# Kernel optimization log

Measured on AMD Instinct MI355X. Metric: run time of the kernel, lower is better.

The kernel has to match this reference:

```python
import jax, jax.numpy as jnp
import numpy as np

N_HEAD, D_HEAD = 10, 38
D_MODEL, D_INNER = 380, 900
QLEN, BSZ = 1024, 4
MIN_LEN, MAX_LEN = -1024, 1024
EPS = 1e-5
SCALE = 1.0 / D_HEAD ** 0.5


def _ln(x, g, b):
    m = x.mean(-1, keepdims=True)
    v = ((x - m) ** 2).mean(-1, keepdims=True)
    return (x - m) / jnp.sqrt(v + EPS) * g + b


def setup_inputs() -> dict:
    key = jax.random.key(0)
    ks = jax.random.split(key, 10)
    s = 0.02
    w = jax.random.normal(ks[0], (QLEN, BSZ, D_MODEL), jnp.float32)
    # sinusoidal relative position embeddings over positions max_len .. min_len
    pos = jnp.arange(MAX_LEN, MIN_LEN - 1, -1, dtype=jnp.float32)  # [rlen]
    inv_freq = 1.0 / (10000.0 ** (jnp.arange(0, D_MODEL, 2, dtype=jnp.float32) / D_MODEL))
    sin_inp = pos[:, None] * inv_freq[None, :]
    r = jnp.concatenate([jnp.sin(sin_inp), jnp.cos(sin_inp)], axis=-1)  # [rlen, d_model]
    # causal mask, True = attend; layout [qlen, klen, bsz]
    attn_mask = jnp.broadcast_to(jnp.tril(jnp.ones((QLEN, QLEN), bool))[:, :, None], (QLEN, QLEN, BSZ))
    attn_relpos = jax.random.randint(ks[1], (BSZ, QLEN, QLEN), MIN_LEN, MAX_LEN + 1).astype(jnp.int32)
    return {
        'w': w,
        'r': r,
        'r_w_bias': s * jax.random.normal(ks[2], (N_HEAD, D_HEAD), jnp.float32),
        'r_r_bias': s * jax.random.normal(ks[3], (N_HEAD, D_HEAD), jnp.float32),
        'qkv_w': s * jax.random.normal(ks[4], (3 * N_HEAD * D_HEAD, D_MODEL), jnp.float32),
        'r_w': s * jax.random.normal(ks[5], (N_HEAD * D_HEAD, D_MODEL), jnp.float32),
        'o_w': s * jax.random.normal(ks[6], (D_MODEL, N_HEAD * D_HEAD), jnp.float32),
        'ln1_g': jnp.ones(D_MODEL, jnp.float32), 'ln1_b': jnp.zeros(D_MODEL, jnp.float32),
        'ff_w1': s * jax.random.normal(ks[7], (D_INNER, D_MODEL), jnp.float32),
        'ff_b1': jnp.zeros(D_INNER, jnp.float32),
        'ff_w2': s * jax.random.normal(ks[8], (D_MODEL, D_INNER), jnp.float32),
        'ff_b2': jnp.zeros(D_MODEL, jnp.float32),
        'ln2_g': jnp.ones(D_MODEL, jnp.float32), 'ln2_b': jnp.zeros(D_MODEL, jnp.float32),
        'attn_mask': attn_mask,
        'attn_relpos': attn_relpos,
        'min_len': MIN_LEN,
        'max_len': MAX_LEN,
    }


def reference(w, r, r_w_bias, r_r_bias, qkv_w, r_w, o_w, ln1_g, ln1_b,
              ff_w1, ff_b1, ff_w2, ff_b2, ln2_g, ln2_b,
              attn_mask, attn_relpos, min_len, max_len):
    qlen, bsz, _ = w.shape
    # qkv projection (no mems, post-lnorm)
    heads = jnp.einsum('ibm,hm->ibh', w, qkv_w)  # [q, b, 3*nh*dh]
    q, k, v = jnp.split(heads, 3, axis=-1)
    q = q.reshape(qlen, bsz, N_HEAD, D_HEAD)
    k = k.reshape(qlen, bsz, N_HEAD, D_HEAD)
    v = v.reshape(qlen, bsz, N_HEAD, D_HEAD)
    rk = (r @ r_w.T).reshape(-1, N_HEAD, D_HEAD)  # [rlen, nh, dh]
    # content score AC and position score BD (Transformer-XL)
    AC = jnp.einsum('ibnd,jbnd->ijbn', q + r_w_bias, k)   # [q, k, b, n]
    BD = jnp.einsum('ibnd,jnd->ijbn', q + r_r_bias, rk)   # [q, rlen, b, n]
    # gather-based relative position indexing (attn_relpos path)
    idx = (max_len - jnp.clip(attn_relpos, min_len, max_len)).transpose(1, 2, 0)  # [q, k, b]
    idx4 = jnp.broadcast_to(idx[..., None], idx.shape + (N_HEAD,))
    BD = jnp.take_along_axis(BD, idx4, axis=1)            # [q, k, b, n]
    score = (AC + BD) * SCALE
    score = jnp.where(attn_mask[:, :, :, None], score, -jnp.inf)
    prob = jax.nn.softmax(score, axis=1)
    vec = jnp.einsum('ijbn,jbnd->ibnd', prob, v).reshape(qlen, bsz, N_HEAD * D_HEAD)
    attn_out = vec @ o_w.T
    out = _ln(w + attn_out, ln1_g, ln1_b)
    # position-wise FF, post-lnorm
    core = jax.nn.relu(out @ ff_w1.T + ff_b1) @ ff_w2.T + ff_b2
    return _ln(out + core, ln2_g, ln2_b)
```

## Files before the change

kernel.cpp:

```cpp
#include <hip/hip_runtime.h>
#include <math.h>

#define QLEN 1024
#define BSZ 4
#define NH 10
#define DH 38
#define DM 380
#define DI 900
#define H3 1140
#define RLEN 2049
#define RLP 2112
#define SCALE 0.16222142113076254f

typedef unsigned short ushortt;
typedef __attribute__((ext_vector_type(8))) short short8;
typedef __attribute__((ext_vector_type(4))) float float4v;

__device__ __forceinline__ float bf2f(ushortt u) {
    return __uint_as_float(((unsigned int)u) << 16);
}
__device__ __forceinline__ ushortt f2bf(float f) {
    unsigned int u = __float_as_uint(f);
    u += 0x7fffu + ((u >> 16) & 1u);
    return (ushortt)(u >> 16);
}

__device__ __forceinline__ void convseg(const float* src, ushortt* dst,
                                        int R, int C, int Rp, int Cp,
                                        int tid0, int stride) {
    const int total = Rp * Cp;
    for (int i = tid0; i < total; i += stride) {
        int r = i / Cp, c = i - r * Cp;
        float v = (r < R && c < C) ? src[(size_t)r * C + c] : 0.f;
        dst[i] = f2bf(v);
    }
}

__global__ __launch_bounds__(256)
void prep_all(const float* __restrict__ w,    ushortt* __restrict__ w_bf,
              const float* __restrict__ qkv,  ushortt* __restrict__ qkv_bf,
              const float* __restrict__ r,    ushortt* __restrict__ r_bf,
              const float* __restrict__ rw,   ushortt* __restrict__ rw_bf,
              const float* __restrict__ ow,   ushortt* __restrict__ ow_bf,
              const float* __restrict__ f1,   ushortt* __restrict__ f1_bf,
              const float* __restrict__ f2,   ushortt* __restrict__ f2_bf,
              ushortt* __restrict__ qw_bf, ushortt* __restrict__ Kb, ushortt* __restrict__ Vb,
              ushortt* __restrict__ qr_bf, ushortt* __restrict__ rk_bf,
              ushortt* __restrict__ vec) {
    const int stride = gridDim.x * 256;
    const int tid0 = blockIdx.x * 256 + threadIdx.x;
    convseg(w,   w_bf,   4096, DM, 4096, 384, tid0, stride);
    convseg(qkv, qkv_bf, H3,   DM, 1152, 384, tid0, stride);
    convseg(r,   r_bf,   RLEN, DM, 2176, 384, tid0, stride);
    convseg(rw,  rw_bf,  DM,   DM, 384,  384, tid0, stride);
    convseg(ow,  ow_bf,  DM,   DM, 384,  384, tid0, stride);
    convseg(f1,  f1_bf,  DI,   DM, 960,  384, tid0, stride);
    convseg(f2,  f2_bf,  DM,   DI, 384,  928, tid0, stride);
    for (int i = tid0; i < BSZ * NH * 1024 * 2; i += stride) {
        size_t idx = (size_t)(i >> 1) * 40 + 38 + (i & 1);
        Kb[idx] = 0; Vb[idx] = 0;
    }
    for (int i = tid0; i < 4096 * 4; i += stride)
        vec[(size_t)(i >> 2) * 384 + 380 + (i & 3)] = 0;
    for (int i = tid0; i < BSZ * NH * 1024 * 26; i += stride) {
        int row = i / 26, c = 38 + i % 26;
        qr_bf[(size_t)row * 64 + c] = 0;
        qw_bf[(size_t)row * 64 + c] = 0;
    }
    for (int i = tid0; i < NH * RLP * 26; i += stride) {
        int row = i / 26, c = 38 + i % 26;
        rk_bf[(size_t)row * 64 + c] = 0;
    }
    for (int i = tid0; i < NH * 63 * 64; i += stride) {
        int n = i / (63 * 64), rem = i % (63 * 64);
        rk_bf[((size_t)n * RLP + RLEN + rem / 64) * 64 + rem % 64] = 0;
    }
}

template<int EPI>
__global__ __launch_bounds__(256)
void gemm_mfma(const ushortt* __restrict__ A, const ushortt* __restrict__ B,
               const float* __restrict__ bias, void* __restrict__ Cout,
               int M, int N, int Kpp, int ldc,
               const float* __restrict__ bias2, float* __restrict__ out2,
               float* __restrict__ out3, float* __restrict__ out4) {
    __shared__ __align__(16) ushortt As[128 * 32];
    __shared__ __align__(16) ushortt Bs[64 * 32];
    const int tid = threadIdx.x;
    const int wid = tid >> 6, lane = tid & 63;
    const int bRow = blockIdx.y * 128, bCol = blockIdx.x * 64;

    float4v acc[2][4];
    const float4v zz = {0.f, 0.f, 0.f, 0.f};
    #pragma unroll
    for (int m = 0; m < 2; ++m)
        #pragma unroll
        for (int n = 0; n < 4; ++n) acc[m][n] = zz;

    const int arow = tid >> 1, acol = (tid & 1) * 16;
    const int brow = tid >> 2, bcol = (tid & 3) * 8;
    const int fr = lane & 15, kg = lane >> 4;

    for (int k0 = 0; k0 < Kpp; k0 += 32) {
        const ushortt* ag = A + (size_t)(bRow + arow) * Kpp + k0 + acol;
        float4v a0 = *(const float4v*)ag;
        float4v a1 = *(const float4v*)(ag + 8);
        const ushortt* bg = B + (size_t)(bCol + brow) * Kpp + k0 + bcol;
        float4v b0 = *(const float4v*)bg;
        __syncthreads();
        *(float4v*)&As[arow * 32 + acol] = a0;
        *(float4v*)&As[arow * 32 + acol + 8] = a1;
        *(float4v*)&Bs[brow * 32 + bcol] = b0;
        __syncthreads();

        short8 bf[4];
        #pragma unroll
        for (int n = 0; n < 4; ++n)
            bf[n] = *(const short8*)&Bs[(n * 16 + fr) * 32 + kg * 8];
        #pragma unroll
        for (int m = 0; m < 2; ++m) {
            short8 af = *(const short8*)&As[(wid * 32 + m * 16 + fr) * 32 + kg * 8];
            #pragma unroll
            for (int n = 0; n < 4; ++n)
                acc[m][n] = __builtin_amdgcn_mfma_f32_16x16x32_bf16(af, bf[n], acc[m][n], 0, 0, 0);
        }
    }

    #pragma unroll
    for (int m = 0; m < 2; ++m)
        #pragma unroll
        for (int n = 0; n < 4; ++n)
            #pragma unroll
            for (int j = 0; j < 4; ++j) {
                const int row = bRow + wid * 32 + m * 16 + (lane >> 4) * 4 + j;
                const int col = bCol + n * 16 + (lane & 15);
                const float v = acc[m][n][j];
                if (EPI == 0) {
                    if (row < M && col < N) ((float*)Cout)[(size_t)row * ldc + col] = v;
                } else if (EPI == 3) {
                    if (row < M && col < 928) {
                        float h = (col < DI) ? fmaxf(v + bias[col], 0.f) : 0.f;
                        ((ushortt*)Cout)[(size_t)row * 928 + col] = f2bf(h);
                    }
                } else if (EPI == 4) {
                    if (row < M && col < N) ((float*)Cout)[(size_t)row * ldc + col] = v + bias[col];
                } else if (EPI == 5) {
                    if (col < H3) {
                        int part = col / 380;
                        int c = col - part * 380;
                        int nh = c / 38, d = c - nh * 38;
                        int q = row >> 2, b2 = row & 3;
                        size_t i40 = (((size_t)b2 * NH + nh) * 1024 + q) * 40 + d;
                        size_t i64 = (((size_t)b2 * NH + nh) * 1024 + q) * 64 + d;
                        if (part == 0) {
                            ((ushortt*)Cout)[i64] = f2bf(v + bias[c]);
                            ((ushortt*)out2)[i64] = f2bf(v + bias2[c]);
                        } else if (part == 1) ((ushortt*)out3)[i40] = f2bf(v);
                        else ((ushortt*)out4)[i40] = f2bf(v);
                    }
                } else {
                    if (row < RLEN && col < DM) {
                        int nh = col / 38, d = col - nh * 38;
                        ((ushortt*)Cout)[((size_t)nh * RLP + row) * 64 + d] = f2bf(v);
                    }
                }
            }
}

__global__ __launch_bounds__(256)
void bd_gemm(const ushortt* __restrict__ qr, const ushortt* __restrict__ rk,
             ushortt* __restrict__ BD, int bofs, int nb) {
    __shared__ __align__(16) ushortt As[64][72];
    __shared__ __align__(16) ushortt Bs[32][72];
    __shared__ __align__(16) ushortt Call[64 * 32 * 10];
    const int bid = blockIdx.x;
    const int xcd = bid & 7, t = bid >> 3;
    const int gl = t / 65, jt = t - gl * 65;
    const int G = gl * 8 + xcd;
    const int lb = G >> 4, qt = G & 15;
    const int tid = threadIdx.x;
    const int wid = tid >> 6, lane = tid & 63;
    const int j0 = jt * 32, q0 = qt * 64;
    const int fr = lane & 15, kg = lane >> 4;
    const int jcount = min(32, RLEN - j0);

    for (int n = 0; n < NH; ++n) {
        const ushortt* Ab = qr + (((size_t)(bofs + lb) * NH + n) * 1024 + q0) * 64;
        const ushortt* Bb = rk + ((size_t)n * RLP + j0) * 64;
        __syncthreads();
        {
            int rr = tid >> 2, cc = (tid & 3) * 16;
            *(float4v*)&As[rr][cc] = *(const float4v*)(Ab + (size_t)rr * 64 + cc);
            *(float4v*)&As[rr][cc + 8] = *(const float4v*)(Ab + (size_t)rr * 64 + cc + 8);
            int br = tid >> 3, bc = (tid & 7) * 8;
            *(float4v*)&Bs[br][bc] = *(const float4v*)(Bb + (size_t)br * 64 + bc);
        }
        __syncthreads();
        float4v acc[2] = {{0.f,0.f,0.f,0.f},{0.f,0.f,0.f,0.f}};
        #pragma unroll
        for (int ks = 0; ks < 64; ks += 32) {
            short8 af = *(const short8*)&As[wid * 16 + fr][ks + kg * 8];
            #pragma unroll
            for (int c = 0; c < 2; ++c) {
                short8 bfr = *(const short8*)&Bs[c * 16 + fr][ks + kg * 8];
                acc[c] = __builtin_amdgcn_mfma_f32_16x16x32_bf16(af, bfr, acc[c], 0, 0, 0);
            }
        }
        #pragma unroll
        for (int c = 0; c < 2; ++c)
            #pragma unroll
            for (int jj = 0; jj < 4; ++jj) {
                int rq = wid * 16 + (lane >> 4) * 4 + jj;
                int cj = c * 16 + (lane & 15);
                Call[(rq * 32 + cj) * 10 + n] = f2bf(acc[c][jj]);
            }
    }
    __syncthreads();
    const int rowdw = jcount * 5;
    const unsigned* Cdw = (const unsigned*)Call;
    unsigned* G2 = (unsigned*)BD;
    for (int idx = tid; idx < 64 * rowdw; idx += 256) {
        int rr = idx / rowdw, rem = idx - rr * rowdw;
        size_t gdw = ((((size_t)lb * 1024 + q0 + rr) * RLEN + j0) * 10) / 2 + rem;
        G2[gdw] = Cdw[rr * 160 + rem];
    }
}

__global__ __launch_bounds__(256)
void attn6(const ushortt* __restrict__ qwb, const ushortt* __restrict__ Kp,
           const ushortt* __restrict__ Vp, const ushortt* __restrict__ BD,
           const int* __restrict__ relpos,
           ushortt* __restrict__ op, float2* __restrict__ ml, int b0, int nb) {
    const int bid = blockIdx.x;
    const int xcd = bid & 7, t = bid >> 3;
    const int gl = t / 10, n = t - gl * 10;
    const int G = gl * 8 + xcd;
    int qc, lb, s;
    {
        const int c3 = 32 * nb, c2 = 24 * nb, c1 = 16 * nb;
        if (G < c3)                { qc = 31 - G / (4 * nb); int r2 = G % (4 * nb); lb = r2 >> 2; s = r2 & 3; }
        else if (G < c3 + c2)      { int l2 = G - c3; qc = 23 - l2 / (3 * nb); int r2 = l2 % (3 * nb); lb = r2 / 3; s = r2 % 3; }
        else if (G < c3 + c2 + c1) { int l2 = G - c3 - c2; qc = 15 - l2 / (2 * nb); int r2 = l2 % (2 * nb); lb = r2 >> 1; s = r2 & 1; }
        else                       { int l2 = G - c3 - c2 - c1; qc = 7 - l2 / nb; lb = l2 % nb; s = 0; }
    }
    const int ns = (qc >> 3) + 1;
    const int qbase = qc * 32;
    const int b = b0 + lb;
    const int tid = threadIdx.x;
    const int wid = tid >> 6, lane = tid & 63;
    const int row = tid >> 3, kg = tid & 7;
    const int qi = qbase + row;
    const size_t bn = (size_t)b * NH + n;
    const size_t prow = ((size_t)s * (BSZ * NH) + bn) * 1024 + qi;
    const int ntiles = (qbase + 95) >> 6;

    __shared__ __align__(16) ushortt KtL[64 * 72];
    __shared__ __align__(16) float   VtL[64 * 40];
    __shared__ __align__(16) ushortt qwL[32 * 72];
    __shared__ __align__(16) ushortt sL[32 * 66];

    const ushortt* Kbase = Kp + bn * 1024 * 40;
    const ushortt* Vbase = Vp + bn * 1024 * 40;
    const int fr = lane & 15;
    const int kg8 = (lane >> 4) * 8;

    {
        int r = tid >> 3, c = (tid & 7) * 8;
        *(short8*)&qwL[r * 72 + c] = *(const short8*)(qwb + (bn * 1024 + qbase + r) * 64 + c);
        for (int i = tid; i < 64 * 24; i += 256) {
            int rr = i / 24, cc = 40 + i % 24;
            KtL[rr * 72 + cc] = 0;
        }
    }
    float o[5] = {0.f, 0.f, 0.f, 0.f, 0.f};
    float mrun = -INFINITY, lrun = 0.f;
    const int* rp = relpos + ((size_t)b * QLEN + qi) * QLEN;
    const ushortt* bdrow = BD + (((size_t)lb * 1024 + qi) * RLEN) * NH + n;

    for (int kt = s; kt < ntiles; kt += ns) {
        const int k0 = kt * 64;
        __syncthreads();
        for (int e = tid; e < 320; e += 256) {
            int rr = e / 5, cc = (e % 5) * 8;
            *(short8*)&KtL[rr * 72 + cc] = *(const short8*)(Kbase + (size_t)(k0 + rr) * 40 + cc);
        }
        {
            const short8* vs = (const short8*)(Vbase + (size_t)k0 * 40);
            for (int e = tid; e < 320; e += 256) {
                short8 vv = vs[e];
                float4v v0v, v1v;
                #pragma unroll
                for (int x = 0; x < 4; ++x) {
                    v0v[x] = bf2f((ushortt)vv[x]); v1v[x] = bf2f((ushortt)vv[4 + x]);
                }
                ((float4v*)VtL)[e * 2] = v0v; ((float4v*)VtL)[e * 2 + 1] = v1v;
            }
        }
        __syncthreads();

        int jv[8];
        #pragma unroll
        for (int ss = 0; ss < 8; ++ss) {
            const int kk = k0 + kg + ss * 8;
            int j = -1;
            if (kk <= qi) {
                int rpv = rp[kk];
                rpv = rpv < -1024 ? -1024 : (rpv > 1024 ? 1024 : rpv);
                j = 1024 - rpv;
            }
            jv[ss] = j;
        }
        float bdv[8];
        #pragma unroll
        for (int ss = 0; ss < 8; ++ss)
            bdv[ss] = (jv[ss] >= 0) ? bf2f(bdrow[(size_t)jv[ss] * NH]) : 0.f;

        {
            const int mt = wid >> 1, ctb = (wid & 1) * 2;
            short8 a0 = *(const short8*)&qwL[(mt * 16 + fr) * 72 + kg8];
            short8 a1 = *(const short8*)&qwL[(mt * 16 + fr) * 72 + 32 + kg8];
            #pragma unroll
            for (int c = 0; c < 2; ++c) {
                const int ct = ctb + c;
                short8 b0f = *(const short8*)&KtL[(ct * 16 + fr) * 72 + kg8];
                short8 b1f = *(const short8*)&KtL[(ct * 16 + fr) * 72 + 32 + kg8];
                float4v acc = {0.f, 0.f, 0.f, 0.f};
                acc = __builtin_amdgcn_mfma_f32_16x16x32_bf16(a0, b0f, acc, 0, 0, 0);
                acc = __builtin_amdgcn_mfma_f32_16x16x32_bf16(a1, b1f, acc, 0, 0, 0);
                #pragma unroll
                for (int j = 0; j < 4; ++j)
                    sL[(mt * 16 + (lane >> 4) * 4 + j) * 66 + ct * 16 + fr] = f2bf(acc[j]);
            }
        }
        __syncthreads();

        float sarr[8];
        float pmax = -INFINITY;
        #pragma unroll
        for (int ss = 0; ss < 8; ++ss) {
            float sv = -INFINITY;
            if (jv[ss] >= 0)
                sv = (bf2f(sL[row * 66 + kg + ss * 8]) + bdv[ss]) * SCALE;
            sarr[ss] = sv;
            pmax = fmaxf(pmax, sv);
        }
        pmax = fmaxf(pmax, __shfl_xor(pmax, 1, 64));
        pmax = fmaxf(pmax, __shfl_xor(pmax, 2, 64));
        pmax = fmaxf(pmax, __shfl_xor(pmax, 4, 64));
        const float nm = fmaxf(mrun, pmax);
        const float corr = __expf(mrun - nm);
        float psum = 0.f;
        ushortt* prw = sL + row * 66;
        #pragma unroll
        for (int ss = 0; ss < 8; ++ss) {
            float p = __expf(sarr[ss] - nm);
            psum += p;
            prw[kg + ss * 8] = f2bf(p);
        }
        psum += __shfl_xor(psum, 1, 64);
        psum += __shfl_xor(psum, 2, 64);
        psum += __shfl_xor(psum, 4, 64);
        lrun = lrun * corr + psum;
        mrun = nm;
        #pragma unroll
        for (int jj = 0; jj < 5; ++jj) o[jj] *= corr;
        int kmax = qi - k0 + 1; if (kmax > 64) kmax = 64;
        #pragma unroll 4
        for (int k = 0; k < kmax; ++k) {
            float p = bf2f(prw[k]);
            const float* vr = VtL + k * 40;
            float4v v4 = *(const float4v*)(vr + 4 * kg);
            float v1 = vr[32 + kg];
            o[0] += p * v4[0]; o[1] += p * v4[1];
            o[2] += p * v4[2]; o[3] += p * v4[3];
            o[4] += p * v1;
        }
    }
    ushortt* oprow = op + prow * 40;
    #pragma unroll
    for (int jj = 0; jj < 4; ++jj) oprow[4 * kg + jj] = f2bf(o[jj]);
    oprow[32 + kg] = f2bf(o[4]);
    if (kg == 0) ml[prow] = make_float2(mrun, lrun);
}

__global__ __launch_bounds__(256)
void attn_combine(const ushortt* __restrict__ op, const float2* __restrict__ ml,
                  ushortt* __restrict__ vec) {
    const int idx = blockIdx.x * 256 + threadIdx.x;
    if (idx >= BSZ * NH * 1024 * 38) return;
    const int d = idx % 38;
    const int rh = idx / 38;
    const int q = rh & 1023;
    const int bn = rh >> 10;
    const int b = bn / NH, n = bn - b * NH;
    const int ns = ((q >> 5) >> 3) + 1;
    const size_t stride = (size_t)BSZ * NH * 1024;
    float M = -INFINITY;
    float2 mv[4];
    for (int sp = 0; sp < ns; ++sp) {
        mv[sp] = ml[sp * stride + rh];
        M = fmaxf(M, mv[sp].x);
    }
    float l = 0.f, o = 0.f;
    for (int sp = 0; sp < ns; ++sp) {
        float w = __expf(mv[sp].x - M);
        l += mv[sp].y * w;
        o += bf2f(op[(sp * stride + rh) * 40 + d]) * w;
    }
    vec[((size_t)q * BSZ + b) * 384 + (size_t)n * 38 + d] = f2bf(o / l);
}

template<bool WRITE_BF>
__global__ __launch_bounds__(256)
void ln_kernel(const float* __restrict__ x1, const float* __restrict__ x2,
               const float* __restrict__ g, const float* __restrict__ bb,
               float* __restrict__ outf, ushortt* __restrict__ outbf) {
    const int row = blockIdx.x;
    const float* p1 = x1 + (size_t)row * DM;
    const float* p2 = x2 + (size_t)row * DM;
    __shared__ float xb[DM];
    __shared__ float red[256];
    const int tid = threadIdx.x;
    float s = 0.f;
    for (int i = tid; i < DM; i += 256) { float v = p1[i] + p2[i]; xb[i] = v; s += v; }
    red[tid] = s; __syncthreads();
    for (int st = 128; st > 0; st >>= 1) { if (tid < st) red[tid] += red[tid + st]; __syncthreads(); }
    const float mean = red[0] / DM;
    __syncthreads();
    float s2 = 0.f;
    for (int i = tid; i < DM; i += 256) { float d = xb[i] - mean; s2 += d * d; }
    red[tid] = s2; __syncthreads();
    for (int st = 128; st > 0; st >>= 1) { if (tid < st) red[tid] += red[tid + st]; __syncthreads(); }
    const float rstd = rsqrtf(red[0] / DM + 1e-5f);
    for (int i = tid; i < (WRITE_BF ? 384 : DM); i += 256) {
        float v = 0.f;
        if (i < DM) {
            v = (xb[i] - mean) * rstd * g[i] + bb[i];
            outf[(size_t)row * DM + i] = v;
        }
        if (WRITE_BF) outbf[(size_t)row * 384 + i] = f2bf(i < DM ? v : 0.f);
    }
}

extern "C" void kernel_launch(void* const* d_in, const int* in_sizes, int n_in,
                              void* d_out, int out_size, void* d_ws, size_t ws_size,
                              hipStream_t stream) {
    const float* w     = (const float*)d_in[0];
    const float* r     = (const float*)d_in[1];
    const float* rwb   = (const float*)d_in[2];
    const float* rrb   = (const float*)d_in[3];
    const float* qkv_w = (const float*)d_in[4];
    const float* r_w   = (const float*)d_in[5];
    const float* o_w   = (const float*)d_in[6];
    const float* ln1g  = (const float*)d_in[7];
    const float* ln1b  = (const float*)d_in[8];
    const float* ffw1  = (const float*)d_in[9];
    const float* ffb1  = (const float*)d_in[10];
    const float* ffw2  = (const float*)d_in[11];
    const float* ffb2  = (const float*)d_in[12];
    const float* ln2g  = (const float*)d_in[13];
    const float* ln2b  = (const float*)d_in[14];
    const int*   relpos = (const int*)d_in[16];
    float* out = (float*)d_out;

    char* cur = (char*)d_ws;
    auto alloc = [&](size_t bytes) { char* p = cur; cur += (bytes + 255) & ~(size_t)255; return p; };
    ushortt* w_bf    = (ushortt*)alloc((size_t)4096 * 384 * 2);
    ushortt* qkv_bf  = (ushortt*)alloc((size_t)1152 * 384 * 2);
    ushortt* r_bf    = (ushortt*)alloc((size_t)2176 * 384 * 2);
    ushortt* rw_bf   = (ushortt*)alloc((size_t)384 * 384 * 2);
    ushortt* ow_bf   = (ushortt*)alloc((size_t)384 * 384 * 2);
    ushortt* f1_bf   = (ushortt*)alloc((size_t)960 * 384 * 2);
    ushortt* f2_bf   = (ushortt*)alloc((size_t)384 * 928 * 2);
    ushortt* qw_bf   = (ushortt*)alloc((size_t)BSZ * NH * 1024 * 64 * 2);
    ushortt* K_bf    = (ushortt*)alloc((size_t)BSZ * NH * 1024 * 40 * 2);
    ushortt* V_bf    = (ushortt*)alloc((size_t)BSZ * NH * 1024 * 40 * 2);
    ushortt* qr_bf   = (ushortt*)alloc((size_t)BSZ * NH * 1024 * 64 * 2);
    ushortt* rk_bf   = (ushortt*)alloc((size_t)NH * RLP * 64 * 2);
    ushortt* vec_bf  = (ushortt*)alloc((size_t)4096 * 384 * 2);
    ushortt* out1_bf = (ushortt*)alloc((size_t)4096 * 384 * 2);
    ushortt* h1_bf   = (ushortt*)alloc((size_t)4096 * 928 * 2);
    float*   attnf   = (float*)alloc((size_t)4096 * DM * 4);
    float*   out1f   = (float*)alloc((size_t)4096 * DM * 4);
    float*   core    = (float*)alloc((size_t)4096 * DM * 4);

    ushortt* op_part = (ushortt*)attnf;
    float2*  ml_part = (float2*)((char*)attnf + (size_t)4 * BSZ * NH * 1024 * 40 * 2);

    const size_t bd_b_bytes = (size_t)1024 * RLEN * NH * 2;
    ushortt* BD = (ushortt*)alloc(bd_b_bytes * BSZ);
    bool full = ((size_t)(cur - (char*)d_ws) <= ws_size);
    if (!full) { cur = (char*)BD; BD = (ushortt*)alloc(bd_b_bytes); }

    auto cgrid = [](size_t total) { return dim3((unsigned)((total + 255) / 256)); };
    prep_all<<<dim3(2048), 256, 0, stream>>>(w, w_bf, qkv_w, qkv_bf, r, r_bf,
                                             r_w, rw_bf, o_w, ow_bf, ffw1, f1_bf, ffw2, f2_bf,
                                             qw_bf, K_bf, V_bf, qr_bf, rk_bf, vec_bf);

    gemm_mfma<5><<<dim3(18, 32), 256, 0, stream>>>(w_bf, qkv_bf, rwb, qw_bf, 4096, H3, 384, 0,
                                                   rrb, (float*)qr_bf, (float*)K_bf, (float*)V_bf);
    gemm_mfma<6><<<dim3(6, 17), 256, 0, stream>>>(r_bf, rw_bf, nullptr, rk_bf, RLEN, DM, 384, 0,
                                                  nullptr, nullptr, nullptr, nullptr);
    if (full) {
        bd_gemm<<<dim3(65 * 16 * BSZ), 256, 0, stream>>>(qr_bf, rk_bf, BD, 0, BSZ);
        attn6<<<dim3(3200), 256, 0, stream>>>(qw_bf, K_bf, V_bf, BD, relpos,
                                              op_part, ml_part, 0, BSZ);
    } else {
        for (int b = 0; b < BSZ; ++b) {
            bd_gemm<<<dim3(65 * 16), 256, 0, stream>>>(qr_bf, rk_bf, BD, b, 1);
            attn6<<<dim3(800), 256, 0, stream>>>(qw_bf, K_bf, V_bf, BD, relpos,
                                                 op_part, ml_part, b, 1);
        }
    }
    attn_combine<<<cgrid((size_t)BSZ * NH * 1024 * 38), 256, 0, stream>>>(op_part, ml_part, vec_bf);
    gemm_mfma<0><<<dim3(6, 32), 256, 0, stream>>>(vec_bf, ow_bf, nullptr, attnf, 4096, DM, 384, DM,
                                                  nullptr, nullptr, nullptr, nullptr);
    ln_kernel<true><<<4096, 256, 0, stream>>>(w, attnf, ln1g, ln1b, out1f, out1_bf);
    gemm_mfma<3><<<dim3(15, 32), 256, 0, stream>>>(out1_bf, f1_bf, ffb1, h1_bf, 4096, DI, 384, 928,
                                                   nullptr, nullptr, nullptr, nullptr);
    gemm_mfma<4><<<dim3(6, 32), 256, 0, stream>>>(h1_bf, f2_bf, ffb2, core, 4096, DM, 928, DM,
                                                  nullptr, nullptr, nullptr, nullptr);
    ln_kernel<false><<<4096, 256, 0, stream>>>(out1f, core, ln2g, ln2b, out, nullptr);
}
```

Baseline: 378.7 us.

## Store BD scores as fp8 e4m3 and shrink attention K/Q/V tile layouts

The materialized position-score tensor BD moves from bf16 to a software-encoded fp8 e4m3 format, with a padded row stride so tiles can be written as aligned dwords. This halves the bytes written by bd_gemm and gathered by the attention kernel. The q_w buffer and the K/V shared-memory tiles shrink from 64/72-wide to 40/48-wide padded rows, and V stays bf16 in LDS instead of being widened to float. The risk is extra accuracy loss from 3-bit-mantissa position scores, plus conversion overhead in the inner loops.

```diff
diff --git a/kernel.cpp b/kernel.cpp
--- a/kernel.cpp
+++ b/kernel.cpp
@@ -10,9 +10,11 @@
 #define H3 1140
 #define RLEN 2049
 #define RLP 2112
+#define RLD 2052
 #define SCALE 0.16222142113076254f
 
 typedef unsigned short ushortt;
+typedef unsigned char uchar;
 typedef __attribute__((ext_vector_type(8))) short short8;
 typedef __attribute__((ext_vector_type(4))) float float4v;
 
@@ -23,6 +25,22 @@
     unsigned int u = __float_as_uint(f);
     u += 0x7fffu + ((u >> 16) & 1u);
     return (ushortt)(u >> 16);
+}
+__device__ __forceinline__ uchar f2e4m3(float f) {
+    unsigned u = __float_as_uint(f);
+    unsigned s = (u >> 24) & 0x80u;
+    unsigned b = u & 0x7fffffffu;
+    b += 0x7FFFFu + ((b >> 20) & 1u);
+    int E = (int)(b >> 23) - 120;
+    if (E <= 0) return (uchar)s;
+    if (E > 15 || (E == 15 && ((b >> 20) & 7u) > 6u)) return (uchar)(s | 0x7Eu);
+    return (uchar)(s | ((unsigned)E << 3) | ((b >> 20) & 7u));
+}
+__device__ __forceinline__ float e4m32f(uchar v) {
+    unsigned s = ((unsigned)(v & 0x80u)) << 24;
+    int E = (v >> 3) & 15; unsigned m = v & 7u;
+    if (E == 0) return __uint_as_float(s);
+    return __uint_as_float(s | ((unsigned)(E + 120) << 23) | (m << 20));
 }
 
 __device__ __forceinline__ void convseg(const float* src, ushortt* dst,
@@ -58,14 +76,13 @@
     convseg(f2,  f2_bf,  DM,   DI, 384,  928, tid0, stride);
     for (int i = tid0; i < BSZ * NH * 1024 * 2; i += stride) {
         size_t idx = (size_t)(i >> 1) * 40 + 38 + (i & 1);
-        Kb[idx] = 0; Vb[idx] = 0;
+        qw_bf[idx] = 0; Kb[idx] = 0; Vb[idx] = 0;
     }
     for (int i = tid0; i < 4096 * 4; i += stride)
         vec[(size_t)(i >> 2) * 384 + 380 + (i & 3)] = 0;
     for (int i = tid0; i < BSZ * NH * 1024 * 26; i += stride) {
         int row = i / 26, c = 38 + i % 26;
         qr_bf[(size_t)row * 64 + c] = 0;
-        qw_bf[(size_t)row * 64 + c] = 0;
     }
     for (int i = tid0; i < NH * RLP * 26; i += stride) {
         int row = i / 26, c = 38 + i % 26;
@@ -153,7 +170,7 @@
                         size_t i40 = (((size_t)b2 * NH + nh) * 1024 + q) * 40 + d;
                         size_t i64 = (((size_t)b2 * NH + nh) * 1024 + q) * 64 + d;
                         if (part == 0) {
-                            ((ushortt*)Cout)[i64] = f2bf(v + bias[c]);
+                            ((ushortt*)Cout)[i40] = f2bf(v + bias[c]);
                             ((ushortt*)out2)[i64] = f2bf(v + bias2[c]);
                         } else if (part == 1) ((ushortt*)out3)[i40] = f2bf(v);
                         else ((ushortt*)out4)[i40] = f2bf(v);
@@ -169,10 +186,10 @@
 
 __global__ __launch_bounds__(256)
 void bd_gemm(const ushortt* __restrict__ qr, const ushortt* __restrict__ rk,
-             ushortt* __restrict__ BD, int bofs, int nb) {
+             uchar* __restrict__ BD, int bofs, int nb) {
     __shared__ __align__(16) ushortt As[64][72];
     __shared__ __align__(16) ushortt Bs[32][72];
-    __shared__ __align__(16) ushortt Call[64 * 32 * 10];
+    __shared__ __align__(16) uchar Call[64 * 32 * 10];
     const int bid = blockIdx.x;
     const int xcd = bid & 7, t = bid >> 3;
     const int gl = t / 65, jt = t - gl * 65;
@@ -212,23 +229,29 @@
             for (int jj = 0; jj < 4; ++jj) {
                 int rq = wid * 16 + (lane >> 4) * 4 + jj;
                 int cj = c * 16 + (lane & 15);
-                Call[(rq * 32 + cj) * 10 + n] = f2bf(acc[c][jj]);
+                Call[(rq * 32 + cj) * 10 + n] = f2e4m3(acc[c][jj]);
             }
     }
     __syncthreads();
-    const int rowdw = jcount * 5;
-    const unsigned* Cdw = (const unsigned*)Call;
-    unsigned* G2 = (unsigned*)BD;
-    for (int idx = tid; idx < 64 * rowdw; idx += 256) {
-        int rr = idx / rowdw, rem = idx - rr * rowdw;
-        size_t gdw = ((((size_t)lb * 1024 + q0 + rr) * RLEN + j0) * 10) / 2 + rem;
-        G2[gdw] = Cdw[rr * 160 + rem];
+    if (jcount == 32) {
+        const unsigned* Cdw = (const unsigned*)Call;
+        unsigned* G2 = (unsigned*)BD;
+        for (int idx = tid; idx < 64 * 80; idx += 256) {
+            int rr = idx / 80, rem = idx - rr * 80;
+            size_t gdw = (((size_t)(lb * 1024 + q0 + rr) * RLD + j0) * 10) >> 2;
+            G2[gdw + rem] = Cdw[rr * 80 + rem];
+        }
+    } else {
+        for (int idx = tid; idx < 64 * 10; idx += 256) {
+            int rr = idx / 10, n2 = idx - rr * 10;
+            BD[((size_t)(lb * 1024 + q0 + rr) * RLD + j0) * 10 + n2] = Call[rr * 320 + n2];
+        }
     }
 }
 
 __global__ __launch_bounds__(256)
-void attn6(const ushortt* __restrict__ qwb, const ushortt* __restrict__ Kp,
-           const ushortt* __restrict__ Vp, const ushortt* __restrict__ BD,
+void attn7(const ushortt* __restrict__ qwb, const ushortt* __restrict__ Kp,
+           const ushortt* __restrict__ Vp, const uchar* __restrict__ BD,
            const int* __restrict__ relpos,
            ushortt* __restrict__ op, float2* __restrict__ ml, int b0, int nb) {
     const int bid = blockIdx.x;
@@ -254,48 +277,36 @@
     const size_t prow = ((size_t)s * (BSZ * NH) + bn) * 1024 + qi;
     const int ntiles = (qbase + 95) >> 6;
 
-    __shared__ __align__(16) ushortt KtL[64 * 72];
-    __shared__ __align__(16) float   VtL[64 * 40];
-    __shared__ __align__(16) ushortt qwL[32 * 72];
+    __shared__ __align__(16) ushortt KtL[64 * 48];
+    __shared__ __align__(16) ushortt VtL[64 * 40];
+    __shared__ __align__(16) ushortt qwL[32 * 48];
     __shared__ __align__(16) ushortt sL[32 * 66];
 
     const ushortt* Kbase = Kp + bn * 1024 * 40;
     const ushortt* Vbase = Vp + bn * 1024 * 40;
     const int fr = lane & 15;
     const int kg8 = (lane >> 4) * 8;
-
-    {
-        int r = tid >> 3, c = (tid & 7) * 8;
-        *(short8*)&qwL[r * 72 + c] = *(const short8*)(qwb + (bn * 1024 + qbase + r) * 64 + c);
-        for (int i = tid; i < 64 * 24; i += 256) {
-            int rr = i / 24, cc = 40 + i % 24;
-            KtL[rr * 72 + cc] = 0;
-        }
+    const bool kgz = (lane >> 4) == 0;
+    const short8 z8 = {0, 0, 0, 0, 0, 0, 0, 0};
+
+    for (int e = tid; e < 160; e += 256) {
+        int rr = e / 5, cc = (e % 5) * 8;
+        *(short8*)&qwL[rr * 48 + cc] = *(const short8*)(qwb + (bn * 1024 + qbase + rr) * 40 + cc);
     }
     float o[5] = {0.f, 0.f, 0.f, 0.f, 0.f};
     float mrun = -INFINITY, lrun = 0.f;
     const int* rp = relpos + ((size_t)b * QLEN + qi) * QLEN;
-    const ushortt* bdrow = BD + (((size_t)lb * 1024 + qi) * RLEN) * NH + n;
+    const uchar* bdrow = BD + ((size_t)(lb * 1024 + qi)) * (RLD * 10) + n;
 
     for (int kt = s; kt < ntiles; kt += ns) {
         const int k0 = kt * 64;
         __syncthreads();
         for (int e = tid; e < 320; e += 256) {
             int rr = e / 5, cc = (e % 5) * 8;
-            *(short8*)&KtL[rr * 72 + cc] = *(const short8*)(Kbase + (size_t)(k0 + rr) * 40 + cc);
-        }
-        {
-            const short8* vs = (const short8*)(Vbase + (size_t)k0 * 40);
-            for (int e = tid; e < 320; e += 256) {
-                short8 vv = vs[e];
-                float4v v0v, v1v;
-                #pragma unroll
-                for (int x = 0; x < 4; ++x) {
-                    v0v[x] = bf2f((ushortt)vv[x]); v1v[x] = bf2f((ushortt)vv[4 + x]);
-                }
-                ((float4v*)VtL)[e * 2] = v0v; ((float4v*)VtL)[e * 2 + 1] = v1v;
-            }
-        }
+            *(short8*)&KtL[rr * 48 + cc] = *(const short8*)(Kbase + (size_t)(k0 + rr) * 40 + cc);
+        }
+        for (int e = tid; e < 320; e += 256)
+            ((short8*)VtL)[e] = ((const short8*)(Vbase + (size_t)k0 * 40))[e];
         __syncthreads();
 
         int jv[8];
@@ -313,17 +324,17 @@
         float bdv[8];
         #pragma unroll
         for (int ss = 0; ss < 8; ++ss)
-            bdv[ss] = (jv[ss] >= 0) ? bf2f(bdrow[(size_t)jv[ss] * NH]) : 0.f;
+            bdv[ss] = (jv[ss] >= 0) ? e4m32f(bdrow[(size_t)jv[ss] * 10]) : 0.f;
 
         {
             const int mt = wid >> 1, ctb = (wid & 1) * 2;
-            short8 a0 = *(const short8*)&qwL[(mt * 16 + fr) * 72 + kg8];
-            short8 a1 = *(const short8*)&qwL[(mt * 16 + fr) * 72 + 32 + kg8];
+            short8 a0 = *(const short8*)&qwL[(mt * 16 + fr) * 48 + kg8];
+            short8 a1 = kgz ? *(const short8*)&qwL[(mt * 16 + fr) * 48 + 32] : z8;
             #pragma unroll
             for (int c = 0; c < 2; ++c) {
                 const int ct = ctb + c;
-                short8 b0f = *(const short8*)&KtL[(ct * 16 + fr) * 72 + kg8];
-                short8 b1f = *(const short8*)&KtL[(ct * 16 + fr) * 72 + 32 + kg8];
+                short8 b0f = *(const short8*)&KtL[(ct * 16 + fr) * 48 + kg8];
+                short8 b1f = kgz ? *(const short8*)&KtL[(ct * 16 + fr) * 48 + 32] : z8;
                 float4v acc = {0.f, 0.f, 0.f, 0.f};
                 acc = __builtin_amdgcn_mfma_f32_16x16x32_bf16(a0, b0f, acc, 0, 0, 0);
                 acc = __builtin_amdgcn_mfma_f32_16x16x32_bf16(a1, b1f, acc, 0, 0, 0);
@@ -368,12 +379,13 @@
         #pragma unroll 4
         for (int k = 0; k < kmax; ++k) {
             float p = bf2f(prw[k]);
-            const float* vr = VtL + k * 40;
-            float4v v4 = *(const float4v*)(vr + 4 * kg);
-            float v1 = vr[32 + kg];
-            o[0] += p * v4[0]; o[1] += p * v4[1];
-            o[2] += p * v4[2]; o[3] += p * v4[3];
-            o[4] += p * v1;
+            const ushortt* vr = VtL + k * 40;
+            uint2 v4u = *(const uint2*)(vr + 4 * kg);
+            o[0] += p * bf2f((ushortt)(v4u.x & 0xffff));
+            o[1] += p * bf2f((ushortt)(v4u.x >> 16));
+            o[2] += p * bf2f((ushortt)(v4u.y & 0xffff));
+            o[3] += p * bf2f((ushortt)(v4u.y >> 16));
+            o[4] += p * bf2f(vr[32 + kg]);
         }
     }
     ushortt* oprow = op + prow * 40;
@@ -472,7 +484,7 @@
     ushortt* ow_bf   = (ushortt*)alloc((size_t)384 * 384 * 2);
     ushortt* f1_bf   = (ushortt*)alloc((size_t)960 * 384 * 2);
     ushortt* f2_bf   = (ushortt*)alloc((size_t)384 * 928 * 2);
-    ushortt* qw_bf   = (ushortt*)alloc((size_t)BSZ * NH * 1024 * 64 * 2);
+    ushortt* qw_bf   = (ushortt*)alloc((size_t)BSZ * NH * 1024 * 40 * 2);
     ushortt* K_bf    = (ushortt*)alloc((size_t)BSZ * NH * 1024 * 40 * 2);
     ushortt* V_bf    = (ushortt*)alloc((size_t)BSZ * NH * 1024 * 40 * 2);
     ushortt* qr_bf   = (ushortt*)alloc((size_t)BSZ * NH * 1024 * 64 * 2);
@@ -487,10 +499,10 @@
     ushortt* op_part = (ushortt*)attnf;
     float2*  ml_part = (float2*)((char*)attnf + (size_t)4 * BSZ * NH * 1024 * 40 * 2);
 
-    const size_t bd_b_bytes = (size_t)1024 * RLEN * NH * 2;
-    ushortt* BD = (ushortt*)alloc(bd_b_bytes * BSZ);
+    const size_t bd_b_bytes = (size_t)1024 * RLD * 10;
+    uchar* BD = (uchar*)alloc(bd_b_bytes * BSZ);
     bool full = ((size_t)(cur - (char*)d_ws) <= ws_size);
-    if (!full) { cur = (char*)BD; BD = (ushortt*)alloc(bd_b_bytes); }
+    if (!full) { cur = (char*)BD; BD = (uchar*)alloc(bd_b_bytes); }
 
     auto cgrid = [](size_t total) { return dim3((unsigned)((total + 255) / 256)); };
     prep_all<<<dim3(2048), 256, 0, stream>>>(w, w_bf, qkv_w, qkv_bf, r, r_bf,
@@ -503,12 +515,12 @@
                                                   nullptr, nullptr, nullptr, nullptr);
     if (full) {
         bd_gemm<<<dim3(65 * 16 * BSZ), 256, 0, stream>>>(qr_bf, rk_bf, BD, 0, BSZ);
-        attn6<<<dim3(3200), 256, 0, stream>>>(qw_bf, K_bf, V_bf, BD, relpos,
+        attn7<<<dim3(3200), 256, 0, stream>>>(qw_bf, K_bf, V_bf, BD, relpos,
                                               op_part, ml_part, 0, BSZ);
     } else {
         for (int b = 0; b < BSZ; ++b) {
             bd_gemm<<<dim3(65 * 16), 256, 0, stream>>>(qr_bf, rk_bf, BD, b, 1);
-            attn6<<<dim3(800), 256, 0, stream>>>(qw_bf, K_bf, V_bf, BD, relpos,
+            attn7<<<dim3(800), 256, 0, stream>>>(qw_bf, K_bf, V_bf, BD, relpos,
                                                  op_part, ml_part, b, 1);
         }
     }
```

New measurement: 352.4 us (median of 2 runs). -6.9%, faster.
